# Kernel tuning notes

Hardware: AMD Instinct MI355X
Metric: run time of the kernel (lower is better)

The kernel has to match this reference:

```python
import jax, jax.numpy as jnp
import numpy as np

B, S, H, D = 8, 1024, 16, 64  # batch, seq, heads, d_heads; hidden = H*D = 1024

def setup_inputs() -> dict:
    key = jax.random.key(0)
    ks = jax.random.split(key, 7)
    sc = 1.0 / np.sqrt(D)
    return {
        "sequences": jax.random.normal(ks[0], (B, S, H * D), dtype=jnp.float32),
        "Wq": jax.random.normal(ks[1], (H, D, D), dtype=jnp.float32) * sc,
        "bq": jax.random.normal(ks[2], (H, D), dtype=jnp.float32) * 0.01,
        "Wk": jax.random.normal(ks[3], (H, D, D), dtype=jnp.float32) * sc,
        "bk": jax.random.normal(ks[4], (H, D), dtype=jnp.float32) * 0.01,
        "Wv": jax.random.normal(ks[5], (H, D, D), dtype=jnp.float32) * sc,
        "bv": jax.random.normal(ks[6], (H, D), dtype=jnp.float32) * 0.01,
    }

def reference(sequences, Wq, bq, Wk, bk, Wv, bv):
    # sequences: [B, S, H*D] -> [B, S, H, D] (head h uses slice h*D:(h+1)*D)
    x = sequences.reshape(B, S, H, D)
    # per-head Linear: y = x @ W.T + b  (torch convention)
    q = jnp.einsum("bshd,hed->bshe", x, Wq) + bq
    k = jnp.einsum("bshd,hed->bshe", x, Wk) + bk
    v = jnp.einsum("bshd,hed->bshe", x, Wv) + bv
    scores = jnp.einsum("bqhd,bkhd->bhqk", q, k) / jnp.sqrt(jnp.float32(D))
    attn = jax.nn.softmax(scores, axis=-1)
    out = jnp.einsum("bhqk,bkhd->bqhd", attn, v)  # [B, S, H, D]
    return out.reshape(B, S, H * D)  # hstack over heads == reshape
```

## Files before the change

### kernel.cpp

```cpp
#include <hip/hip_runtime.h>
#include <hip/hip_bf16.h>


typedef __attribute__((ext_vector_type(8))) short short8;
typedef __attribute__((ext_vector_type(4))) float f32x4;
typedef __attribute__((ext_vector_type(16))) float f32x16;
typedef __attribute__((ext_vector_type(2))) unsigned int u32x2;
typedef __attribute__((ext_vector_type(4))) unsigned int u32x4;

#define MFMA16 __builtin_amdgcn_mfma_f32_16x16x32_bf16
#define MFMA32 __builtin_amdgcn_mfma_f32_32x32x16_bf16

#define QSCALE 0.1803368801111204f

__device__ __forceinline__ unsigned cvt_pk(float lo, float hi) {
  unsigned r;
  asm("v_cvt_pk_bf16_f32 %0, %1, %2" : "=v"(r) : "v"(lo), "v"(hi));
  return r;
}
__device__ __forceinline__ void pl32_swap(unsigned &a, unsigned &b) {
  asm("v_permlane32_swap_b32 %0, %1" : "+v"(a), "+v"(b));
}
__device__ __forceinline__ u32x2 pk4(const f32x4 v) {
  return (u32x2){cvt_pk(v[0], v[1]), cvt_pk(v[2], v[3])};
}
__device__ __forceinline__ void pack_cd(const f32x16& p, short8& lo, short8& hi8) {
  unsigned d0 = cvt_pk(p[0],  p[1]);
  unsigned d2 = cvt_pk(p[4],  p[5]);
  pl32_swap(d0, d2);
  unsigned d1 = cvt_pk(p[2],  p[3]);
  unsigned d3 = cvt_pk(p[6],  p[7]);
  pl32_swap(d1, d3);
  u32x4 a = {d0, d1, d2, d3};
  unsigned e0 = cvt_pk(p[8],  p[9]);
  unsigned e2 = cvt_pk(p[12], p[13]);
  pl32_swap(e0, e2);
  unsigned e1 = cvt_pk(p[10], p[11]);
  unsigned e3 = cvt_pk(p[14], p[15]);
  pl32_swap(e1, e3);
  u32x4 b = {e0, e1, e2, e3};
  lo  = __builtin_bit_cast(short8, a);
  hi8 = __builtin_bit_cast(short8, b);
}
__device__ __forceinline__ void lds_barrier() {
  asm volatile("s_waitcnt lgkmcnt(0)" ::: "memory");
  __builtin_amdgcn_s_barrier();
}

__global__ __launch_bounds__(256) void kv_proj_kernel(
    const float* __restrict__ x,
    const float* __restrict__ Wk, const float* __restrict__ bk,
    const float* __restrict__ Wv, const float* __restrict__ bv,
    unsigned short* __restrict__ kv_ws)
{
  __shared__ unsigned short x_lds[64][72];
  __shared__ unsigned short w_lds[2][64][72];

  const int h   = blockIdx.x & 15;
  const int tb  = blockIdx.x >> 4;
  const int tid = threadIdx.x;
  const int w   = tid >> 6;
  const int l   = tid & 63;
  const int hi  = l >> 5;
  const int cc  = l & 31;

  {
    const int i  = tid >> 2;
    const int q4 = tid & 3;
    const float* xs  = x  + (size_t)(tb * 64 + i) * 1024 + h * 64 + q4 * 16;
    const float* wsk = Wk + (size_t)h * 4096 + i * 64 + q4 * 16;
    const float* wsv = Wv + (size_t)h * 4096 + i * 64 + q4 * 16;
#pragma unroll
    for (int it = 0; it < 4; ++it) {
      const int c = q4 * 16 + it * 4;
      *(u32x2*)&x_lds[i][c]    = pk4(*(const f32x4*)(xs  + it * 4));
      *(u32x2*)&w_lds[0][i][c] = pk4(*(const f32x4*)(wsk + it * 4));
      *(u32x2*)&w_lds[1][i][c] = pk4(*(const f32x4*)(wsv + it * 4));
    }
  }
  __syncthreads();

  const int b = tb >> 4;
  unsigned short* kvt = kv_ws + (size_t)(b * 16 + h) * 131072
                              + (size_t)(tb & 15) * 8192;

  {
    const int eb = w >> 1, cb = w & 1;
    f32x16 kkT = {};
#pragma unroll
    for (int ks = 0; ks < 4; ++ks) {
      short8 aW = *(const short8*)&w_lds[0][eb * 32 + cc][ks * 16 + hi * 8];
      short8 bX = *(const short8*)&x_lds[cb * 32 + cc][ks * 16 + hi * 8];
      kkT = MFMA32(aW, bX, kkT, 0, 0, 0);
    }
    const float* bkb = bk + h * 64 + eb * 32 + 4 * hi;
    f32x4 bk0 = *(const f32x4*)(bkb);
    f32x4 bk1 = *(const f32x4*)(bkb + 8);
    f32x4 bk2 = *(const f32x4*)(bkb + 16);
    f32x4 bk3 = *(const f32x4*)(bkb + 24);
#pragma unroll
    for (int r = 0; r < 16; ++r) {
      const float bb = (r >> 2) == 0 ? bk0[r & 3] :
                       (r >> 2) == 1 ? bk1[r & 3] :
                       (r >> 2) == 2 ? bk2[r & 3] : bk3[r & 3];
      kkT[r] += bb;
    }
    short8 klo, khi;
    pack_cd(kkT, klo, khi);
    const int slot = 256 * eb + 64 * cb + 32 * hi + cc;
    *(short8*)&kvt[slot * 8]         = klo;
    *(short8*)&kvt[(slot + 128) * 8] = khi;
  }

  {
    const int tb32 = w >> 1, db = w & 1;
    f32x16 vvC = {};
#pragma unroll
    for (int ks = 0; ks < 4; ++ks) {
      short8 aX = *(const short8*)&x_lds[tb32 * 32 + cc][ks * 16 + hi * 8];
      short8 bW = *(const short8*)&w_lds[1][db * 32 + cc][ks * 16 + hi * 8];
      vvC = MFMA32(aX, bW, vvC, 0, 0, 0);
    }
    const float bvv = bv[h * 64 + db * 32 + cc];
#pragma unroll
    for (int r = 0; r < 16; ++r) vvC[r] += bvv;
    short8 vlo, vhi;
    pack_cd(vvC, vlo, vhi);
    const int slot = 256 * tb32 + 64 * db + 32 * hi + cc;
    *(short8*)&kvt[4096 + slot * 8]         = vlo;
    *(short8*)&kvt[4096 + (slot + 128) * 8] = vhi;
  }
}

__global__ __launch_bounds__(512, 4) void attn_kernel(
    const float* __restrict__ x,
    const float* __restrict__ Wq, const float* __restrict__ bq,
    const unsigned short* __restrict__ kv_ws,
    float* __restrict__ out)
{
  __shared__ __align__(16) char lds[32768];

  const int logical = (blockIdx.x & 7) * 64 + (blockIdx.x >> 3);
  const int qt = logical & 3;
  const int bh = logical >> 2;
  const int b  = bh >> 4;
  const int h  = bh & 15;
  const unsigned short* kvb = kv_ws + (size_t)bh * 131072;

  const int tid = threadIdx.x;
  const int w   = tid >> 6;
  const int l   = tid & 63;
  const int hi  = l >> 5;
  const int cc  = l & 31;

  const unsigned short* sgp = kvb + tid * 8;
  char* wbp = lds + tid * 16;

  short8 st[2];
#pragma unroll
  for (int j = 0; j < 2; ++j) st[j] = *(const short8*)(sgp + j * 4096);

  unsigned short* wq_l = (unsigned short*)lds;
  unsigned short* xh_l = (unsigned short*)(lds + 9216);

  {
    const int r = tid >> 3, s = tid & 7;
    const float* ws = Wq + h * 4096 + r * 64 + s * 8;
    f32x4 v0 = *(const f32x4*)ws;
    f32x4 v1 = *(const f32x4*)(ws + 4);
    u32x4 d = {cvt_pk(v0[0], v0[1]), cvt_pk(v0[2], v0[3]),
               cvt_pk(v1[0], v1[1]), cvt_pk(v1[2], v1[3])};
    *(u32x4*)&wq_l[r * 72 + s * 8] = d;
  }

  short8 qf[4];
  f32x16 qa0 = {}, qa1 = {};
#pragma unroll
  for (int p = 0; p < 2; ++p) {
    {
      const int r = tid >> 2, s = tid & 3;
      const float* xs = x + ((size_t)(b * 1024 + qt * 256 + p * 128 + r)) * 1024
                          + h * 64 + s * 16;
      f32x4 v0 = *(const f32x4*)xs;
      f32x4 v1 = *(const f32x4*)(xs + 4);
      f32x4 v2 = *(const f32x4*)(xs + 8);
      f32x4 v3 = *(const f32x4*)(xs + 12);
      u32x4 d0 = {cvt_pk(v0[0], v0[1]), cvt_pk(v0[2], v0[3]),
                  cvt_pk(v1[0], v1[1]), cvt_pk(v1[2], v1[3])};
      u32x4 d1 = {cvt_pk(v2[0], v2[1]), cvt_pk(v2[2], v2[3]),
                  cvt_pk(v3[0], v3[1]), cvt_pk(v3[2], v3[3])};
      *(u32x4*)&xh_l[r * 72 + s * 16]     = d0;
      *(u32x4*)&xh_l[r * 72 + s * 16 + 8] = d1;
    }
    lds_barrier();
    if ((w >> 2) == p) {
      const int tl = (w & 3) * 32 + cc;
#pragma unroll
      for (int c = 0; c < 4; ++c) {
        short8 xf  = *(const short8*)&xh_l[tl * 72 + c * 16 + hi * 8];
        short8 alo = *(const short8*)&wq_l[cc * 72 + c * 16 + hi * 8];
        short8 ahi = *(const short8*)&wq_l[(32 + cc) * 72 + c * 16 + hi * 8];
        qa0 = MFMA32(alo, xf, qa0, 0, 0, 0);
        qa1 = MFMA32(ahi, xf, qa1, 0, 0, 0);
      }
    }
    lds_barrier();
  }
  {
#pragma unroll
    for (int r = 0; r < 16; ++r) {
      const int e = (r & 3) + 8 * (r >> 2) + 4 * hi;
      qa0[r] = (qa0[r] + bq[h * 64 + e]) * QSCALE;
      qa1[r] = (qa1[r] + bq[h * 64 + 32 + e]) * QSCALE;
    }
    pack_cd(qa0, qf[0], qf[1]);
    pack_cd(qa1, qf[2], qf[3]);
  }

#pragma unroll
  for (int j = 0; j < 2; ++j) *(short8*)(wbp + j * 8192) = st[j];
#pragma unroll
  for (int j = 0; j < 2; ++j) st[j] = *(const short8*)(sgp + 8192 + j * 4096);
  lds_barrier();

  f32x16 ot0 = {}; f32x16 ot1 = {};
  float lsum = 0.f;

  for (int kv = 0; kv < 16; ++kv) {
    if (kv < 15) {
      char* d = wbp + ((kv + 1) & 1) * 16384;
#pragma unroll
      for (int j = 0; j < 2; ++j) *(short8*)(d + j * 8192) = st[j];
      if (kv < 14) {
        const unsigned short* s = sgp + (size_t)(kv + 2) * 8192;
#pragma unroll
        for (int j = 0; j < 2; ++j) st[j] = *(const short8*)(s + j * 4096);
      }
    }
    const char* kb_ = lds + (kv & 1) * 16384;
    const char* vb_ = kb_ + 8192;

    f32x16 s0 = {}; f32x16 s1 = {};
    __builtin_amdgcn_s_setprio(1);
#pragma unroll
    for (int c = 0; c < 4; ++c) {
      s0 = MFMA32(*(const short8*)(kb_ + (c * 128 + l) * 16),      qf[c], s0, 0, 0, 0);
      s1 = MFMA32(*(const short8*)(kb_ + (c * 128 + 64 + l) * 16), qf[c], s1, 0, 0, 0);
    }
    __builtin_amdgcn_s_setprio(0);

    float ps0 = 0.f, ps1 = 0.f;
#pragma unroll
    for (int i = 0; i < 16; ++i) { s0[i] = __builtin_amdgcn_exp2f(s0[i]); ps0 += s0[i]; }
#pragma unroll
    for (int i = 0; i < 16; ++i) { s1[i] = __builtin_amdgcn_exp2f(s1[i]); ps1 += s1[i]; }
    lsum += ps0 + ps1;

#pragma unroll
    for (int kb = 0; kb < 2; ++kb) {
      short8 pa0, pa1;
      pack_cd(kb ? s1 : s0, pa0, pa1);

      const int c20 = kb * 2, c21 = kb * 2 + 1;
      __builtin_amdgcn_s_setprio(1);
      ot0 = MFMA32(*(const short8*)(vb_ + (c20 * 128 + l) * 16),      pa0, ot0, 0, 0, 0);
      ot1 = MFMA32(*(const short8*)(vb_ + (c20 * 128 + 64 + l) * 16), pa0, ot1, 0, 0, 0);
      ot0 = MFMA32(*(const short8*)(vb_ + (c21 * 128 + l) * 16),      pa1, ot0, 0, 0, 0);
      ot1 = MFMA32(*(const short8*)(vb_ + (c21 * 128 + 64 + l) * 16), pa1, ot1, 0, 0, 0);
      __builtin_amdgcn_s_setprio(0);
    }
    lds_barrier();
  }

  const float lt  = lsum + __shfl_xor(lsum, 32, 64);
  const float inv = 1.0f / lt;
  const int s_row = qt * 256 + w * 32 + cc;
  float* op = out + ((size_t)(b * 1024 + s_row) << 10) + h * 64;
#pragma unroll
  for (int rg = 0; rg < 4; ++rg) {
    const int d0 = 8 * rg + 4 * hi;
    f32x4 v0, v1;
#pragma unroll
    for (int j = 0; j < 4; ++j) {
      v0[j] = ot0[rg * 4 + j] * inv;
      v1[j] = ot1[rg * 4 + j] * inv;
    }
    *(f32x4*)(op + d0)      = v0;
    *(f32x4*)(op + 32 + d0) = v1;
  }
}

extern "C" void kernel_launch(void* const* d_in, const int* in_sizes, int n_in,
                              void* d_out, int out_size, void* d_ws, size_t ws_size,
                              hipStream_t stream) {
  const float* x  = (const float*)d_in[0];
  const float* Wq = (const float*)d_in[1];
  const float* bq = (const float*)d_in[2];
  const float* Wk = (const float*)d_in[3];
  const float* bk = (const float*)d_in[4];
  const float* Wv = (const float*)d_in[5];
  const float* bv = (const float*)d_in[6];
  float* out = (float*)d_out;

  unsigned short* kv_ws = (unsigned short*)d_ws;

  kv_proj_kernel<<<2048, 256, 0, stream>>>(x, Wk, bk, Wv, bv, kv_ws);
  attn_kernel<<<512, 512, 0, stream>>>(x, Wq, bq, kv_ws, out);
}
```

Measured before the change: 70.56 us.

## Fuse K/V projection into attention kernel, recomputing per query tile

Removes the separate K/V projection kernel and its bf16 workspace round trip. Each attention block now streams raw fp32 x tiles into LDS, projects them to K and V with MFMA, and feeds them straight to the attention loop, double-buffered across iterations. This saves a kernel launch and the workspace write and read, but each K/V tile is recomputed by all four query-tile blocks of a head. It also uses more LDS (48KB), which may lower occupancy.

```diff
diff --git a/kernel.cpp b/kernel.cpp
--- a/kernel.cpp
+++ b/kernel.cpp
@@ -5,10 +5,8 @@
 typedef __attribute__((ext_vector_type(8))) short short8;
 typedef __attribute__((ext_vector_type(4))) float f32x4;
 typedef __attribute__((ext_vector_type(16))) float f32x16;
-typedef __attribute__((ext_vector_type(2))) unsigned int u32x2;
 typedef __attribute__((ext_vector_type(4))) unsigned int u32x4;
 
-#define MFMA16 __builtin_amdgcn_mfma_f32_16x16x32_bf16
 #define MFMA32 __builtin_amdgcn_mfma_f32_32x32x16_bf16
 
 #define QSCALE 0.1803368801111204f
@@ -21,8 +19,12 @@
 __device__ __forceinline__ void pl32_swap(unsigned &a, unsigned &b) {
   asm("v_permlane32_swap_b32 %0, %1" : "+v"(a), "+v"(b));
 }
-__device__ __forceinline__ u32x2 pk4(const f32x4 v) {
-  return (u32x2){cvt_pk(v[0], v[1]), cvt_pk(v[2], v[3])};
+__device__ __forceinline__ short8 ld8bf(const float* p) {
+  f32x4 v0 = *(const f32x4*)p;
+  f32x4 v1 = *(const f32x4*)(p + 4);
+  u32x4 d = {cvt_pk(v0[0], v0[1]), cvt_pk(v0[2], v0[3]),
+             cvt_pk(v1[0], v1[1]), cvt_pk(v1[2], v1[3])};
+  return __builtin_bit_cast(short8, d);
 }
 __device__ __forceinline__ void pack_cd(const f32x16& p, short8& lo, short8& hi8) {
   unsigned d0 = cvt_pk(p[0],  p[1]);
@@ -42,123 +44,27 @@
   lo  = __builtin_bit_cast(short8, a);
   hi8 = __builtin_bit_cast(short8, b);
 }
-__device__ __forceinline__ void lds_barrier() {
-  asm volatile("s_waitcnt lgkmcnt(0)" ::: "memory");
-  __builtin_amdgcn_s_barrier();
-}
-
-__global__ __launch_bounds__(256) void kv_proj_kernel(
+
+__global__ __launch_bounds__(512, 4) void fused_msa_kernel(
     const float* __restrict__ x,
+    const float* __restrict__ Wq, const float* __restrict__ bq,
     const float* __restrict__ Wk, const float* __restrict__ bk,
     const float* __restrict__ Wv, const float* __restrict__ bv,
-    unsigned short* __restrict__ kv_ws)
+    float* __restrict__ out)
 {
-  __shared__ unsigned short x_lds[64][72];
-  __shared__ unsigned short w_lds[2][64][72];
-
-  const int h   = blockIdx.x & 15;
-  const int tb  = blockIdx.x >> 4;
+  __shared__ __align__(16) char lds[49152];
+
+  const int logical = (blockIdx.x & 7) * 64 + (blockIdx.x >> 3);
+  const int qt = logical & 3;
+  const int bh = logical >> 2;
+  const int b  = bh >> 4;
+  const int h  = bh & 15;
+
   const int tid = threadIdx.x;
   const int w   = tid >> 6;
   const int l   = tid & 63;
   const int hi  = l >> 5;
   const int cc  = l & 31;
-
-  {
-    const int i  = tid >> 2;
-    const int q4 = tid & 3;
-    const float* xs  = x  + (size_t)(tb * 64 + i) * 1024 + h * 64 + q4 * 16;
-    const float* wsk = Wk + (size_t)h * 4096 + i * 64 + q4 * 16;
-    const float* wsv = Wv + (size_t)h * 4096 + i * 64 + q4 * 16;
-#pragma unroll
-    for (int it = 0; it < 4; ++it) {
-      const int c = q4 * 16 + it * 4;
-      *(u32x2*)&x_lds[i][c]    = pk4(*(const f32x4*)(xs  + it * 4));
-      *(u32x2*)&w_lds[0][i][c] = pk4(*(const f32x4*)(wsk + it * 4));
-      *(u32x2*)&w_lds[1][i][c] = pk4(*(const f32x4*)(wsv + it * 4));
-    }
-  }
-  __syncthreads();
-
-  const int b = tb >> 4;
-  unsigned short* kvt = kv_ws + (size_t)(b * 16 + h) * 131072
-                              + (size_t)(tb & 15) * 8192;
-
-  {
-    const int eb = w >> 1, cb = w & 1;
-    f32x16 kkT = {};
-#pragma unroll
-    for (int ks = 0; ks < 4; ++ks) {
-      short8 aW = *(const short8*)&w_lds[0][eb * 32 + cc][ks * 16 + hi * 8];
-      short8 bX = *(const short8*)&x_lds[cb * 32 + cc][ks * 16 + hi * 8];
-      kkT = MFMA32(aW, bX, kkT, 0, 0, 0);
-    }
-    const float* bkb = bk + h * 64 + eb * 32 + 4 * hi;
-    f32x4 bk0 = *(const f32x4*)(bkb);
-    f32x4 bk1 = *(const f32x4*)(bkb + 8);
-    f32x4 bk2 = *(const f32x4*)(bkb + 16);
-    f32x4 bk3 = *(const f32x4*)(bkb + 24);
-#pragma unroll
-    for (int r = 0; r < 16; ++r) {
-      const float bb = (r >> 2) == 0 ? bk0[r & 3] :
-                       (r >> 2) == 1 ? bk1[r & 3] :
-                       (r >> 2) == 2 ? bk2[r & 3] : bk3[r & 3];
-      kkT[r] += bb;
-    }
-    short8 klo, khi;
-    pack_cd(kkT, klo, khi);
-    const int slot = 256 * eb + 64 * cb + 32 * hi + cc;
-    *(short8*)&kvt[slot * 8]         = klo;
-    *(short8*)&kvt[(slot + 128) * 8] = khi;
-  }
-
-  {
-    const int tb32 = w >> 1, db = w & 1;
-    f32x16 vvC = {};
-#pragma unroll
-    for (int ks = 0; ks < 4; ++ks) {
-      short8 aX = *(const short8*)&x_lds[tb32 * 32 + cc][ks * 16 + hi * 8];
-      short8 bW = *(const short8*)&w_lds[1][db * 32 + cc][ks * 16 + hi * 8];
-      vvC = MFMA32(aX, bW, vvC, 0, 0, 0);
-    }
-    const float bvv = bv[h * 64 + db * 32 + cc];
-#pragma unroll
-    for (int r = 0; r < 16; ++r) vvC[r] += bvv;
-    short8 vlo, vhi;
-    pack_cd(vvC, vlo, vhi);
-    const int slot = 256 * tb32 + 64 * db + 32 * hi + cc;
-    *(short8*)&kvt[4096 + slot * 8]         = vlo;
-    *(short8*)&kvt[4096 + (slot + 128) * 8] = vhi;
-  }
-}
-
-__global__ __launch_bounds__(512, 4) void attn_kernel(
-    const float* __restrict__ x,
-    const float* __restrict__ Wq, const float* __restrict__ bq,
-    const unsigned short* __restrict__ kv_ws,
-    float* __restrict__ out)
-{
-  __shared__ __align__(16) char lds[32768];
-
-  const int logical = (blockIdx.x & 7) * 64 + (blockIdx.x >> 3);
-  const int qt = logical & 3;
-  const int bh = logical >> 2;
-  const int b  = bh >> 4;
-  const int h  = bh & 15;
-  const unsigned short* kvb = kv_ws + (size_t)bh * 131072;
-
-  const int tid = threadIdx.x;
-  const int w   = tid >> 6;
-  const int l   = tid & 63;
-  const int hi  = l >> 5;
-  const int cc  = l & 31;
-
-  const unsigned short* sgp = kvb + tid * 8;
-  char* wbp = lds + tid * 16;
-
-  short8 st[2];
-#pragma unroll
-  for (int j = 0; j < 2; ++j) st[j] = *(const short8*)(sgp + j * 4096);
 
   unsigned short* wq_l = (unsigned short*)lds;
   unsigned short* xh_l = (unsigned short*)(lds + 9216);
@@ -192,7 +98,7 @@
       *(u32x4*)&xh_l[r * 72 + s * 16]     = d0;
       *(u32x4*)&xh_l[r * 72 + s * 16 + 8] = d1;
     }
-    lds_barrier();
+    __syncthreads();
     if ((w >> 2) == p) {
       const int tl = (w & 3) * 32 + cc;
 #pragma unroll
@@ -204,7 +110,7 @@
         qa1 = MFMA32(ahi, xf, qa1, 0, 0, 0);
       }
     }
-    lds_barrier();
+    __syncthreads();
   }
   {
 #pragma unroll
@@ -217,27 +123,122 @@
     pack_cd(qa1, qf[2], qf[3]);
   }
 
-#pragma unroll
-  for (int j = 0; j < 2; ++j) *(short8*)(wbp + j * 8192) = st[j];
-#pragma unroll
-  for (int j = 0; j < 2; ++j) st[j] = *(const short8*)(sgp + 8192 + j * 4096);
-  lds_barrier();
+  short8 wst[4];
+  {
+    const float* Wsrc = (w < 4) ? Wk : Wv;
+    const int wrb = (w < 4) ? (w >> 1) : ((w - 4) & 1);
+    const float* wp = Wsrc + h * 4096 + (wrb * 32 + cc) * 64 + hi * 8;
+#pragma unroll
+    for (int ks = 0; ks < 4; ++ks) wst[ks] = ld8bf(wp + ks * 16);
+  }
+  f32x4 bk0, bk1, bk2, bk3;
+  if (w < 4) {
+    const float* bkb = bk + h * 64 + (w >> 1) * 32 + 4 * hi;
+    bk0 = *(const f32x4*)(bkb);
+    bk1 = *(const f32x4*)(bkb + 8);
+    bk2 = *(const f32x4*)(bkb + 16);
+    bk3 = *(const f32x4*)(bkb + 24);
+  }
+
+  const int xrow = tid >> 3;
+  const int xseg = tid & 7;
+  const float* xsg = x + ((size_t)(b * 1024 + xrow)) * 1024 + h * 64 + xseg * 8;
+  const int xslot = 128 * (xseg >> 1) + 64 * (xrow >> 5) + 32 * (xseg & 1) + (xrow & 31);
+  char* xw = lds + 32768 + xslot * 16;
+
+#pragma unroll
+  for (int t0 = 0; t0 < 2; ++t0) {
+    f32x4 a0 = *(const f32x4*)(xsg + (size_t)t0 * 65536);
+    f32x4 a1 = *(const f32x4*)(xsg + (size_t)t0 * 65536 + 4);
+    u32x4 d = {cvt_pk(a0[0], a0[1]), cvt_pk(a0[2], a0[3]),
+               cvt_pk(a1[0], a1[1]), cvt_pk(a1[2], a1[3])};
+    *(u32x4*)(xw + t0 * 8192) = d;
+  }
+  __syncthreads();
+
+  {
+    const char* xbuf = lds + 32768;
+    char* fdst = lds;
+    if (w < 4) {
+      const int eb = w >> 1, cb = w & 1;
+      f32x16 kk = {};
+#pragma unroll
+      for (int ks = 0; ks < 4; ++ks)
+        kk = MFMA32(wst[ks], *(const short8*)(xbuf + (128 * ks + 64 * cb + l) * 16), kk, 0, 0, 0);
+#pragma unroll
+      for (int r = 0; r < 16; ++r) {
+        const float bb = (r >> 2) == 0 ? bk0[r & 3] :
+                         (r >> 2) == 1 ? bk1[r & 3] :
+                         (r >> 2) == 2 ? bk2[r & 3] : bk3[r & 3];
+        kk[r] += bb;
+      }
+      short8 klo, khi;
+      pack_cd(kk, klo, khi);
+      const int slot = 256 * eb + 64 * cb + l;
+      *(short8*)(fdst + slot * 16)         = klo;
+      *(short8*)(fdst + (slot + 128) * 16) = khi;
+    } else {
+      const int tb32 = (w - 4) >> 1, db = (w - 4) & 1;
+      f32x16 vv = {};
+#pragma unroll
+      for (int ks = 0; ks < 4; ++ks)
+        vv = MFMA32(*(const short8*)(xbuf + (128 * ks + 64 * tb32 + l) * 16), wst[ks], vv, 0, 0, 0);
+      const float bvv = bv[h * 64 + db * 32 + cc];
+#pragma unroll
+      for (int r = 0; r < 16; ++r) vv[r] += bvv;
+      short8 vlo, vhi;
+      pack_cd(vv, vlo, vhi);
+      const int slot = 256 * tb32 + 64 * db + l;
+      *(short8*)(fdst + 8192 + slot * 16)         = vlo;
+      *(short8*)(fdst + 8192 + (slot + 128) * 16) = vhi;
+    }
+  }
+  __syncthreads();
 
   f32x16 ot0 = {}; f32x16 ot1 = {};
   float lsum = 0.f;
 
-  for (int kv = 0; kv < 16; ++kv) {
-    if (kv < 15) {
-      char* d = wbp + ((kv + 1) & 1) * 16384;
-#pragma unroll
-      for (int j = 0; j < 2; ++j) *(short8*)(d + j * 8192) = st[j];
-      if (kv < 14) {
-        const unsigned short* s = sgp + (size_t)(kv + 2) * 8192;
-#pragma unroll
-        for (int j = 0; j < 2; ++j) st[j] = *(const short8*)(s + j * 4096);
+  for (int t = 0; t < 16; ++t) {
+    if (t < 15) {
+      const char* xbuf = lds + 32768 + ((t + 1) & 1) * 8192;
+      char* fdst = lds + ((t + 1) & 1) * 16384;
+      if (w < 4) {
+        const int eb = w >> 1, cb = w & 1;
+        f32x16 kk = {};
+#pragma unroll
+        for (int ks = 0; ks < 4; ++ks)
+          kk = MFMA32(wst[ks], *(const short8*)(xbuf + (128 * ks + 64 * cb + l) * 16), kk, 0, 0, 0);
+#pragma unroll
+        for (int r = 0; r < 16; ++r) {
+          const float bb = (r >> 2) == 0 ? bk0[r & 3] :
+                           (r >> 2) == 1 ? bk1[r & 3] :
+                           (r >> 2) == 2 ? bk2[r & 3] : bk3[r & 3];
+          kk[r] += bb;
+        }
+        short8 klo, khi;
+        pack_cd(kk, klo, khi);
+        const int slot = 256 * eb + 64 * cb + l;
+        *(short8*)(fdst + slot * 16)         = klo;
+        *(short8*)(fdst + (slot + 128) * 16) = khi;
+      } else {
+        const int tb32 = (w - 4) >> 1, db = (w - 4) & 1;
+        f32x16 vv = {};
+#pragma unroll
+        for (int ks = 0; ks < 4; ++ks)
+          vv = MFMA32(*(const short8*)(xbuf + (128 * ks + 64 * tb32 + l) * 16), wst[ks], vv, 0, 0, 0);
+        const float bvv = bv[h * 64 + db * 32 + cc];
+#pragma unroll
+        for (int r = 0; r < 16; ++r) vv[r] += bvv;
+        short8 vlo, vhi;
+        pack_cd(vv, vlo, vhi);
+        const int slot = 256 * tb32 + 64 * db + l;
+        *(short8*)(fdst + 8192 + slot * 16)         = vlo;
+        *(short8*)(fdst + 8192 + (slot + 128) * 16) = vhi;
       }
     }
-    const char* kb_ = lds + (kv & 1) * 16384;
+    __syncthreads();
+
+    const char* kb_ = lds + (t & 1) * 16384;
     const char* vb_ = kb_ + 8192;
 
     f32x16 s0 = {}; f32x16 s1 = {};
@@ -260,7 +261,6 @@
     for (int kb = 0; kb < 2; ++kb) {
       short8 pa0, pa1;
       pack_cd(kb ? s1 : s0, pa0, pa1);
-
       const int c20 = kb * 2, c21 = kb * 2 + 1;
       __builtin_amdgcn_s_setprio(1);
       ot0 = MFMA32(*(const short8*)(vb_ + (c20 * 128 + l) * 16),      pa0, ot0, 0, 0, 0);
@@ -269,7 +269,16 @@
       ot1 = MFMA32(*(const short8*)(vb_ + (c21 * 128 + 64 + l) * 16), pa1, ot1, 0, 0, 0);
       __builtin_amdgcn_s_setprio(0);
     }
-    lds_barrier();
+
+    if (t < 14) {
+      const float* s = xsg + (size_t)(t + 2) * 65536;
+      f32x4 a0 = *(const f32x4*)s;
+      f32x4 a1 = *(const f32x4*)(s + 4);
+      u32x4 d = {cvt_pk(a0[0], a0[1]), cvt_pk(a0[2], a0[3]),
+                 cvt_pk(a1[0], a1[1]), cvt_pk(a1[2], a1[3])};
+      *(u32x4*)(xw + (t & 1) * 8192) = d;
+    }
+    if (t < 15) __syncthreads();
   }
 
   const float lt  = lsum + __shfl_xor(lsum, 32, 64);
@@ -302,8 +311,5 @@
   const float* bv = (const float*)d_in[6];
   float* out = (float*)d_out;
 
-  unsigned short* kv_ws = (unsigned short*)d_ws;
-
-  kv_proj_kernel<<<2048, 256, 0, stream>>>(x, Wk, bk, Wv, bv, kv_ws);
-  attn_kernel<<<512, 512, 0, stream>>>(x, Wq, bq, kv_ws, out);
-}
+  fused_msa_kernel<<<512, 512, 0, stream>>>(x, Wq, bq, Wk, bk, Wv, bv, out);
+}
```

Measured after the change: 77.93 us. 1.1x slower.

## Double K/V projection tile per block and split K and V across warp groups

Applied to the files above, without the earlier changes.

The K/V projection kernel now handles 128 sequence rows per block with 512 threads instead of 64 rows with 256 threads. Wk and Wv are loaded and converted once per 128 rows, which halves the weight reloads, and the grid shrinks to 1024 blocks. Warps 0-3 compute K and warps 4-7 compute V, each over two 64-row subtiles, and global loads and LDS writes are widened to 16 bytes. The tradeoffs are fewer blocks for latency hiding and more LDS per block.

```diff
diff --git a/kernel.cpp b/kernel.cpp
--- a/kernel.cpp
+++ b/kernel.cpp
@@ -8,7 +8,6 @@
 typedef __attribute__((ext_vector_type(2))) unsigned int u32x2;
 typedef __attribute__((ext_vector_type(4))) unsigned int u32x4;
 
-#define MFMA16 __builtin_amdgcn_mfma_f32_16x16x32_bf16
 #define MFMA32 __builtin_amdgcn_mfma_f32_32x32x16_bf16
 
 #define QSCALE 0.1803368801111204f
@@ -20,9 +19,6 @@
 }
 __device__ __forceinline__ void pl32_swap(unsigned &a, unsigned &b) {
   asm("v_permlane32_swap_b32 %0, %1" : "+v"(a), "+v"(b));
-}
-__device__ __forceinline__ u32x2 pk4(const f32x4 v) {
-  return (u32x2){cvt_pk(v[0], v[1]), cvt_pk(v[2], v[3])};
 }
 __device__ __forceinline__ void pack_cd(const f32x16& p, short8& lo, short8& hi8) {
   unsigned d0 = cvt_pk(p[0],  p[1]);
@@ -47,14 +43,15 @@
   __builtin_amdgcn_s_barrier();
 }
 
-__global__ __launch_bounds__(256) void kv_proj_kernel(
+__global__ __launch_bounds__(512) void kv_proj_kernel(
     const float* __restrict__ x,
     const float* __restrict__ Wk, const float* __restrict__ bk,
     const float* __restrict__ Wv, const float* __restrict__ bv,
     unsigned short* __restrict__ kv_ws)
 {
-  __shared__ unsigned short x_lds[64][72];
-  __shared__ unsigned short w_lds[2][64][72];
+  __shared__ unsigned short x_lds[128][72];
+  __shared__ unsigned short wk_lds[64][72];
+  __shared__ unsigned short wv_lds[64][72];
 
   const int h   = blockIdx.x & 15;
   const int tb  = blockIdx.x >> 4;
@@ -65,70 +62,89 @@
   const int cc  = l & 31;
 
   {
-    const int i  = tid >> 2;
-    const int q4 = tid & 3;
-    const float* xs  = x  + (size_t)(tb * 64 + i) * 1024 + h * 64 + q4 * 16;
-    const float* wsk = Wk + (size_t)h * 4096 + i * 64 + q4 * 16;
-    const float* wsv = Wv + (size_t)h * 4096 + i * 64 + q4 * 16;
-#pragma unroll
-    for (int it = 0; it < 4; ++it) {
-      const int c = q4 * 16 + it * 4;
-      *(u32x2*)&x_lds[i][c]    = pk4(*(const f32x4*)(xs  + it * 4));
-      *(u32x2*)&w_lds[0][i][c] = pk4(*(const f32x4*)(wsk + it * 4));
-      *(u32x2*)&w_lds[1][i][c] = pk4(*(const f32x4*)(wsv + it * 4));
-    }
+    const int r = tid >> 2, s = tid & 3;
+    const float* xs = x + (size_t)(tb * 128 + r) * 1024 + h * 64 + s * 16;
+    f32x4 v0 = *(const f32x4*)xs;
+    f32x4 v1 = *(const f32x4*)(xs + 4);
+    f32x4 v2 = *(const f32x4*)(xs + 8);
+    f32x4 v3 = *(const f32x4*)(xs + 12);
+    u32x4 d0 = {cvt_pk(v0[0], v0[1]), cvt_pk(v0[2], v0[3]),
+                cvt_pk(v1[0], v1[1]), cvt_pk(v1[2], v1[3])};
+    u32x4 d1 = {cvt_pk(v2[0], v2[1]), cvt_pk(v2[2], v2[3]),
+                cvt_pk(v3[0], v3[1]), cvt_pk(v3[2], v3[3])};
+    *(u32x4*)&x_lds[r][s * 16]     = d0;
+    *(u32x4*)&x_lds[r][s * 16 + 8] = d1;
+  }
+  {
+    const int r = tid >> 3, s = tid & 7;
+    const float* wsk = Wk + (size_t)h * 4096 + r * 64 + s * 8;
+    const float* wsv = Wv + (size_t)h * 4096 + r * 64 + s * 8;
+    f32x4 k0 = *(const f32x4*)wsk;
+    f32x4 k1 = *(const f32x4*)(wsk + 4);
+    u32x4 dk = {cvt_pk(k0[0], k0[1]), cvt_pk(k0[2], k0[3]),
+                cvt_pk(k1[0], k1[1]), cvt_pk(k1[2], k1[3])};
+    *(u32x4*)&wk_lds[r][s * 8] = dk;
+    f32x4 m0 = *(const f32x4*)wsv;
+    f32x4 m1 = *(const f32x4*)(wsv + 4);
+    u32x4 dv = {cvt_pk(m0[0], m0[1]), cvt_pk(m0[2], m0[3]),
+                cvt_pk(m1[0], m1[1]), cvt_pk(m1[2], m1[3])};
+    *(u32x4*)&wv_lds[r][s * 8] = dv;
   }
   __syncthreads();
 
-  const int b = tb >> 4;
+  const int b = tb >> 3;
   unsigned short* kvt = kv_ws + (size_t)(b * 16 + h) * 131072
-                              + (size_t)(tb & 15) * 8192;
-
-  {
+                              + (size_t)(tb & 7) * 16384;
+
+  if (w < 4) {
     const int eb = w >> 1, cb = w & 1;
-    f32x16 kkT = {};
-#pragma unroll
-    for (int ks = 0; ks < 4; ++ks) {
-      short8 aW = *(const short8*)&w_lds[0][eb * 32 + cc][ks * 16 + hi * 8];
-      short8 bX = *(const short8*)&x_lds[cb * 32 + cc][ks * 16 + hi * 8];
-      kkT = MFMA32(aW, bX, kkT, 0, 0, 0);
-    }
     const float* bkb = bk + h * 64 + eb * 32 + 4 * hi;
     f32x4 bk0 = *(const f32x4*)(bkb);
     f32x4 bk1 = *(const f32x4*)(bkb + 8);
     f32x4 bk2 = *(const f32x4*)(bkb + 16);
     f32x4 bk3 = *(const f32x4*)(bkb + 24);
 #pragma unroll
-    for (int r = 0; r < 16; ++r) {
-      const float bb = (r >> 2) == 0 ? bk0[r & 3] :
-                       (r >> 2) == 1 ? bk1[r & 3] :
-                       (r >> 2) == 2 ? bk2[r & 3] : bk3[r & 3];
-      kkT[r] += bb;
-    }
-    short8 klo, khi;
-    pack_cd(kkT, klo, khi);
-    const int slot = 256 * eb + 64 * cb + 32 * hi + cc;
-    *(short8*)&kvt[slot * 8]         = klo;
-    *(short8*)&kvt[(slot + 128) * 8] = khi;
-  }
-
-  {
-    const int tb32 = w >> 1, db = w & 1;
-    f32x16 vvC = {};
-#pragma unroll
-    for (int ks = 0; ks < 4; ++ks) {
-      short8 aX = *(const short8*)&x_lds[tb32 * 32 + cc][ks * 16 + hi * 8];
-      short8 bW = *(const short8*)&w_lds[1][db * 32 + cc][ks * 16 + hi * 8];
-      vvC = MFMA32(aX, bW, vvC, 0, 0, 0);
-    }
+    for (int sub = 0; sub < 2; ++sub) {
+      f32x16 kkT = {};
+#pragma unroll
+      for (int ks = 0; ks < 4; ++ks) {
+        short8 aW = *(const short8*)&wk_lds[eb * 32 + cc][ks * 16 + hi * 8];
+        short8 bX = *(const short8*)&x_lds[sub * 64 + cb * 32 + cc][ks * 16 + hi * 8];
+        kkT = MFMA32(aW, bX, kkT, 0, 0, 0);
+      }
+#pragma unroll
+      for (int r = 0; r < 16; ++r) {
+        const float bb = (r >> 2) == 0 ? bk0[r & 3] :
+                         (r >> 2) == 1 ? bk1[r & 3] :
+                         (r >> 2) == 2 ? bk2[r & 3] : bk3[r & 3];
+        kkT[r] += bb;
+      }
+      short8 klo, khi;
+      pack_cd(kkT, klo, khi);
+      const int slot = 256 * eb + 64 * cb + l;
+      *(short8*)&kvt[sub * 8192 + slot * 8]         = klo;
+      *(short8*)&kvt[sub * 8192 + (slot + 128) * 8] = khi;
+    }
+  } else {
+    const int tb32 = (w - 4) >> 1, db = (w - 4) & 1;
     const float bvv = bv[h * 64 + db * 32 + cc];
 #pragma unroll
-    for (int r = 0; r < 16; ++r) vvC[r] += bvv;
-    short8 vlo, vhi;
-    pack_cd(vvC, vlo, vhi);
-    const int slot = 256 * tb32 + 64 * db + 32 * hi + cc;
-    *(short8*)&kvt[4096 + slot * 8]         = vlo;
-    *(short8*)&kvt[4096 + (slot + 128) * 8] = vhi;
+    for (int sub = 0; sub < 2; ++sub) {
+      f32x16 vvC = {};
+#pragma unroll
+      for (int ks = 0; ks < 4; ++ks) {
+        short8 aX = *(const short8*)&x_lds[sub * 64 + tb32 * 32 + cc][ks * 16 + hi * 8];
+        short8 bW = *(const short8*)&wv_lds[db * 32 + cc][ks * 16 + hi * 8];
+        vvC = MFMA32(aX, bW, vvC, 0, 0, 0);
+      }
+#pragma unroll
+      for (int r = 0; r < 16; ++r) vvC[r] += bvv;
+      short8 vlo, vhi;
+      pack_cd(vvC, vlo, vhi);
+      const int slot = 256 * tb32 + 64 * db + l;
+      *(short8*)&kvt[sub * 8192 + 4096 + slot * 8]         = vlo;
+      *(short8*)&kvt[sub * 8192 + 4096 + (slot + 128) * 8] = vhi;
+    }
   }
 }
 
@@ -304,6 +320,6 @@
 
   unsigned short* kv_ws = (unsigned short*)d_ws;
 
-  kv_proj_kernel<<<2048, 256, 0, stream>>>(x, Wk, bk, Wv, bv, kv_ws);
+  kv_proj_kernel<<<1024, 512, 0, stream>>>(x, Wk, bk, Wv, bv, kv_ws);
   attn_kernel<<<512, 512, 0, stream>>>(x, Wq, bq, kv_ws, out);
 }
```

New measurement: 67.21 us. -4.7%, faster.
